# Kernel tuning notes

Measured on AMD Instinct MI355X. Metric: run time of the kernel, lower is better.

Reference implementation:

```python
import jax, jax.numpy as jnp
import numpy as np

D_IN = 1024
D_OUT = 1024
SEQ = 2048
BATCH = 4


def setup_inputs() -> dict:
    key = jax.random.key(0)
    ks = jax.random.split(key, 7)
    s_in = 1.0 / np.sqrt(D_IN)
    return {
        "x": jax.random.normal(ks[0], (BATCH, SEQ, D_IN), dtype=jnp.float32),
        "Wq": jax.random.normal(ks[1], (D_IN, D_OUT), dtype=jnp.float32) * s_in,
        "bq": jax.random.normal(ks[2], (D_OUT,), dtype=jnp.float32) * 0.01,
        "Wk": jax.random.normal(ks[3], (D_IN, D_OUT), dtype=jnp.float32) * s_in,
        "bk": jax.random.normal(ks[4], (D_OUT,), dtype=jnp.float32) * 0.01,
        "Wv": jax.random.normal(ks[5], (D_IN, D_OUT), dtype=jnp.float32) * s_in,
        "bv": jax.random.normal(ks[6], (D_OUT,), dtype=jnp.float32) * 0.01,
    }


def reference(x, Wq, bq, Wk, bk, Wv, bv):
    # x: [b, n, d_in]
    b, n, d_in = x.shape
    q = x @ Wq + bq  # [b, n, d_out]
    k = x @ Wk + bk
    v = x @ Wv + bv
    scale = 1.0 / jnp.sqrt(jnp.asarray(d_in, x.dtype))
    scores = jnp.einsum("bqd,bkd->bqk", q, k) * scale  # [b, n, n]
    causal = jnp.triu(jnp.ones((n, n), dtype=bool), k=1)  # True above diagonal
    scores = jnp.where(causal, -jnp.inf, scores)
    weights = jax.nn.softmax(scores, axis=-1)
    # dropout p=0.0 -> identity
    context = jnp.einsum("bqk,bkd->bqd", weights, v)
    return context
```

## Files before the change

### kernel.cpp

```cpp
#include <hip/hip_runtime.h>

typedef unsigned short u16;
typedef __bf16 bf16x8 __attribute__((ext_vector_type(8)));
typedef float floatx4 __attribute__((ext_vector_type(4)));

#define B_ 4
#define SEQ 2048
#define DIM 1024

__device__ __forceinline__ u16 f2bf(float f) {
    unsigned u = __builtin_bit_cast(unsigned, f);
    u += 0x7FFFu + ((u >> 16) & 1u);
    return (u16)(u >> 16);
}
__device__ __forceinline__ float bf2f(u16 h) {
    unsigned u = ((unsigned)h) << 16;
    return __builtin_bit_cast(float, u);
}

#define GPTR(p) ((const __attribute__((address_space(1))) void*)(p))
#define LPTR(p) ((__attribute__((address_space(3))) void*)(p))

__global__ __launch_bounds__(256) void convert_x(const float4* __restrict__ x,
                                                 ushort4* __restrict__ xb) {
    int i = blockIdx.x * 256 + threadIdx.x;
    float4 v = x[i];
    ushort4 o;
    o.x = f2bf(v.x); o.y = f2bf(v.y); o.z = f2bf(v.z); o.w = f2bf(v.w);
    xb[i] = o;
}

__global__ __launch_bounds__(256) void transpose_w(const float* __restrict__ Wq,
                                                   const float* __restrict__ Wk,
                                                   const float* __restrict__ Wv,
                                                   u16* __restrict__ Wt) {
    __shared__ u16 t[64][66];
    const int z = blockIdx.z;
    const float* W = (z == 0) ? Wq : ((z == 1) ? Wk : Wv);
    u16* out = Wt + (size_t)z * DIM * DIM;
    const int tx = threadIdx.x, ty = threadIdx.y;
    const int k0 = blockIdx.x * 64, n0 = blockIdx.y * 64;
#pragma unroll
    for (int j = 0; j < 8; j++) {
        int k = ty + 8 * j;
        float2 v = *(const float2*)(W + (size_t)(k0 + k) * DIM + n0 + 2 * tx);
        t[2 * tx][k] = f2bf(v.x);
        t[2 * tx + 1][k] = f2bf(v.y);
    }
    __syncthreads();
#pragma unroll
    for (int j = 0; j < 8; j++) {
        int n = ty + 8 * j;
        ushort2 o;
        o.x = t[n][2 * tx];
        o.y = t[n][2 * tx + 1];
        *(ushort2*)(out + (size_t)(n0 + n) * DIM + k0 + 2 * tx) = o;
    }
}

__device__ __forceinline__ void mainloop(
    const u16* __restrict__ Ab, const u16* __restrict__ Bb, int lda, int ldb,
    int Kt, u16* lsA, u16* lsB, int tid, int wave, int quad, int l15,
    int wm, int wn, floatx4 (&acc)[4][2]) {
    const int srow = tid >> 2;
    const int scol = ((tid & 3) ^ ((tid >> 3) & 3)) * 8;
    const u16* gA = Ab + (size_t)srow * lda + scol;
    const u16* gB = Bb + (size_t)srow * ldb + scol;
    const int swq = (quad ^ ((l15 >> 1) & 3)) * 8;
    const int rowA = l15 * 32;

#pragma unroll
    for (int i = 0; i < 4; i++)
#pragma unroll
        for (int j = 0; j < 2; j++) {
            floatx4 zz = {0.f, 0.f, 0.f, 0.f};
            acc[i][j] = zz;
        }

    for (int k0 = 0; k0 < Kt; k0 += 64) {
#pragma unroll
        for (int h = 0; h < 2; h++) {
            __builtin_amdgcn_global_load_lds(GPTR(gA + h * 32),
                LPTR(lsA + h * 4096 + wave * 512), 16, 0, 0);
            __builtin_amdgcn_global_load_lds(GPTR(gA + (size_t)64 * lda + h * 32),
                LPTR(lsA + h * 4096 + 2048 + wave * 512), 16, 0, 0);
            __builtin_amdgcn_global_load_lds(GPTR(gB + h * 32),
                LPTR(lsB + h * 2048 + wave * 512), 16, 0, 0);
        }
        gA += 64; gB += 64;
        __syncthreads();

#pragma unroll
        for (int h = 0; h < 2; h++) {
            bf16x8 af[4], bfr[2];
#pragma unroll
            for (int i = 0; i < 4; i++)
                af[i] = *(const bf16x8*)(lsA + h * 4096 + (wm + i * 16) * 32 + rowA + swq);
#pragma unroll
            for (int j = 0; j < 2; j++)
                bfr[j] = *(const bf16x8*)(lsB + h * 2048 + (wn + j * 16) * 32 + rowA + swq);
#pragma unroll
            for (int i = 0; i < 4; i++)
#pragma unroll
                for (int j = 0; j < 2; j++)
                    acc[i][j] = __builtin_amdgcn_mfma_f32_16x16x32_bf16(af[i], bfr[j], acc[i][j], 0, 0, 0);
        }
        __syncthreads();
    }
}

__global__ __launch_bounds__(256, 4) void gemm_qkv(
    const u16* __restrict__ A, const u16* __restrict__ Bt, u16* __restrict__ QK,
    const float* __restrict__ b0, const float* __restrict__ b1, const float* __restrict__ b2,
    u16* __restrict__ VtOut) {
    __shared__ union {
        struct { u16 a[128 * 64]; u16 b[64 * 64]; } stage;
        u16 epT[64 * 136];
    } sm;
    const int tid = threadIdx.x;
    const int wave = tid >> 6, lane = tid & 63;
    const int quad = lane >> 4, l15 = lane & 15;
    const int wm = (wave >> 1) * 64, wn = (wave & 1) * 32;
    const int z = blockIdx.x >> 4, xn = blockIdx.x & 15, yb = blockIdx.y;

    const u16* Ab = A + (size_t)yb * 128 * DIM;
    const u16* Bb = Bt + (size_t)z * DIM * DIM + (size_t)xn * 64 * DIM;
    floatx4 acc[4][2];
    mainloop(Ab, Bb, DIM, DIM, DIM, sm.stage.a, sm.stage.b,
             tid, wave, quad, l15, wm, wn, acc);

    const int colbase = xn * 64;
    const int mq = quad * 4;
    const float* bias = (z == 0) ? b0 : ((z == 1) ? b1 : b2);
    const int n0 = colbase + wn + l15;

    if (z < 2) {
        u16* Cb = QK + (size_t)z * B_ * SEQ * DIM;
        const int m0 = yb * 128 + wm + mq;
#pragma unroll
        for (int j = 0; j < 2; j++) {
            float bv_ = bias[n0 + j * 16];
#pragma unroll
            for (int i = 0; i < 4; i++)
#pragma unroll
                for (int r = 0; r < 4; r++)
                    Cb[(size_t)(m0 + i * 16 + r) * DIM + (n0 + j * 16)] = f2bf(acc[i][j][r] + bv_);
        }
        return;
    }

    float addj[2];
#pragma unroll
    for (int j = 0; j < 2; j++) addj[j] = bias[n0 + j * 16];
    __syncthreads();
#pragma unroll
    for (int i = 0; i < 4; i++)
#pragma unroll
        for (int j = 0; j < 2; j++)
#pragma unroll
            for (int r = 0; r < 4; r++) {
                int lr = wm + i * 16 + mq + r;
                int lc = wn + j * 16 + l15;
                sm.epT[lc * 136 + lr] = f2bf(acc[i][j][r] + addj[j]);
            }
    __syncthreads();
    const int b = (yb * 128) >> 11;
    const int sb = (yb * 128) & (SEQ - 1);
    u16* Vb = VtOut + (size_t)b * DIM * SEQ;
#pragma unroll
    for (int k = 0; k < 4; k++) {
        int s2 = tid + 256 * k;
        int n = s2 >> 4, seg = s2 & 15;
        uint4 val = *(const uint4*)&sm.epT[n * 136 + seg * 8];
        *(uint4*)(Vb + (size_t)(colbase + n) * SEQ + sb + seg * 8) = val;
    }
}

__global__ __launch_bounds__(256, 4) void gemm_scores(
    const u16* __restrict__ Q, const u16* __restrict__ K, u16* __restrict__ S,
    float scale) {
    const int ym = gridDim.y - 1 - blockIdx.y;
    if ((int)blockIdx.x > 2 * ym + 1) return;

    __shared__ u16 lsA[128 * 64];
    __shared__ u16 lsB[64 * 64];
    const int tid = threadIdx.x;
    const int wave = tid >> 6, lane = tid & 63;
    const int quad = lane >> 4, l15 = lane & 15;
    const int wm = (wave >> 1) * 64, wn = (wave & 1) * 32;
    const int z = blockIdx.z;

    const u16* Ab = Q + (size_t)z * SEQ * DIM + (size_t)ym * 128 * DIM;
    const u16* Bb = K + (size_t)z * SEQ * DIM + (size_t)blockIdx.x * 64 * DIM;
    floatx4 acc[4][2];
    mainloop(Ab, Bb, DIM, DIM, DIM, lsA, lsB,
             tid, wave, quad, l15, wm, wn, acc);

    u16* Cb = S + (size_t)z * SEQ * SEQ;
    const int m0 = ym * 128 + wm + quad * 4;
    const int n0 = blockIdx.x * 64 + wn + l15;
#pragma unroll
    for (int j = 0; j < 2; j++)
#pragma unroll
        for (int i = 0; i < 4; i++)
#pragma unroll
            for (int r = 0; r < 4; r++)
                Cb[(size_t)(m0 + i * 16 + r) * SEQ + (n0 + j * 16)] = f2bf(acc[i][j][r] * scale);
}

__global__ __launch_bounds__(256, 4) void gemm_pv(
    const u16* __restrict__ P, const u16* __restrict__ Vt, float* __restrict__ O) {
    const int ym = gridDim.y - 1 - blockIdx.y;
    __shared__ u16 lsA[128 * 64];
    __shared__ u16 lsB[64 * 64];
    const int tid = threadIdx.x;
    const int wave = tid >> 6, lane = tid & 63;
    const int quad = lane >> 4, l15 = lane & 15;
    const int wm = (wave >> 1) * 64, wn = (wave & 1) * 32;
    const int z = blockIdx.z;

    const u16* Ab = P + (size_t)z * SEQ * SEQ + (size_t)ym * 128 * SEQ;
    const u16* Bb = Vt + (size_t)z * DIM * SEQ + (size_t)blockIdx.x * 64 * SEQ;
    const int Kt = (ym + 1) * 128;
    floatx4 acc[4][2];
    mainloop(Ab, Bb, SEQ, SEQ, Kt, lsA, lsB,
             tid, wave, quad, l15, wm, wn, acc);

    float* Cf = O + (size_t)z * SEQ * DIM;
    const int m0 = ym * 128 + wm + quad * 4;
    const int n0 = blockIdx.x * 64 + wn + l15;
#pragma unroll
    for (int j = 0; j < 2; j++)
#pragma unroll
        for (int i = 0; i < 4; i++)
#pragma unroll
            for (int r = 0; r < 4; r++)
                Cf[(size_t)(m0 + i * 16 + r) * DIM + (n0 + j * 16)] = acc[i][j][r];
}

__global__ __launch_bounds__(256) void softmax_causal(u16* __restrict__ S) {
    const int q = blockIdx.x, b = blockIdx.y, tid = threadIdx.x;
    u16* row = S + ((size_t)b * SEQ + q) * SEQ;
    const int L = q + 1;
    const int Z = ((q >> 7) + 1) << 7;
    const int k0 = tid * 8;
    __shared__ float redm[4], reds[4];

    uint4 rv = ((const uint4*)row)[tid];
    unsigned w[4] = {rv.x, rv.y, rv.z, rv.w};
    float f[8];
#pragma unroll
    for (int e = 0; e < 8; e++) {
        u16 h = (u16)((w[e >> 1] >> ((e & 1) * 16)) & 0xFFFFu);
        f[e] = (k0 + e < L) ? bf2f(h) : -3.0e38f;
    }
    float m = f[0];
#pragma unroll
    for (int e = 1; e < 8; e++) m = fmaxf(m, f[e]);
#pragma unroll
    for (int o = 32; o > 0; o >>= 1) m = fmaxf(m, __shfl_xor(m, o));
    if ((tid & 63) == 0) redm[tid >> 6] = m;
    __syncthreads();
    m = fmaxf(fmaxf(redm[0], redm[1]), fmaxf(redm[2], redm[3]));

    float p[8];
    float s = 0.f;
#pragma unroll
    for (int e = 0; e < 8; e++) {
        p[e] = (k0 + e < L) ? __expf(f[e] - m) : 0.f;
        s += p[e];
    }
#pragma unroll
    for (int o = 32; o > 0; o >>= 1) s += __shfl_xor(s, o);
    if ((tid & 63) == 0) reds[tid >> 6] = s;
    __syncthreads();
    s = reds[0] + reds[1] + reds[2] + reds[3];
    const float inv = 1.0f / s;

    if (k0 < Z) {
        unsigned o2[4];
#pragma unroll
        for (int e = 0; e < 4; e++) {
            unsigned lo = f2bf(p[2 * e] * inv);
            unsigned hi = f2bf(p[2 * e + 1] * inv);
            o2[e] = lo | (hi << 16);
        }
        uint4 ov = {o2[0], o2[1], o2[2], o2[3]};
        ((uint4*)row)[tid] = ov;
    }
}

extern "C" void kernel_launch(void* const* d_in, const int* in_sizes, int n_in,
                              void* d_out, int out_size, void* d_ws, size_t ws_size,
                              hipStream_t stream) {
    const float* x = (const float*)d_in[0];
    const float* Wq = (const float*)d_in[1];
    const float* bq = (const float*)d_in[2];
    const float* Wk = (const float*)d_in[3];
    const float* bk = (const float*)d_in[4];
    const float* Wv = (const float*)d_in[5];
    const float* bv = (const float*)d_in[6];
    float* out = (float*)d_out;

    char* ws = (char*)d_ws;
    const size_t MB = 1024ull * 1024ull;
    u16* S = (u16*)ws;
    u16* xb = (u16*)ws;
    u16* Wt = (u16*)(ws + 16 * MB);
    u16* QK = (u16*)(ws + 32 * MB);
    u16* Vt = (u16*)(ws + 64 * MB);
    const size_t MAT = (size_t)B_ * SEQ * DIM;
    u16* Q = QK;
    u16* Km = QK + MAT;

    const float scale = 0.03125f;

    convert_x<<<8192, 256, 0, stream>>>((const float4*)x, (ushort4*)xb);
    transpose_w<<<dim3(16, 16, 3), dim3(32, 8), 0, stream>>>(Wq, Wk, Wv, Wt);
    gemm_qkv<<<dim3(48, 64), 256, 0, stream>>>(xb, Wt, QK, bq, bk, bv, Vt);
    gemm_scores<<<dim3(32, 16, 4), 256, 0, stream>>>(Q, Km, S, scale);
    softmax_causal<<<dim3(SEQ, B_), 256, 0, stream>>>(S);
    gemm_pv<<<dim3(16, 16, 4), 256, 0, stream>>>(S, Vt, out);
}
```

Measured before the change: 282.6 us.

## Enlarge GEMM block tiles to 128x128 with 64x64 per-wave subtiles

All three GEMM kernels move from 128x64 block tiles to 128x128, with each wave computing a 64x64 output subtile (4x4 MFMA accumulators) instead of 64x32. The aim is to raise arithmetic intensity per LDS and global load and halve the number of blocks. The cost is more registers, hence launch bounds lowered to 3 blocks per CU, and larger LDS B buffers. The V-transpose epilogue is split into two passes so it still fits the existing shared buffer.

Result: faster. 249.6 us (-11.7%).

```diff
diff --git a/kernel.cpp b/kernel.cpp
--- a/kernel.cpp
+++ b/kernel.cpp
@@ -61,75 +61,75 @@
 __device__ __forceinline__ void mainloop(
     const u16* __restrict__ Ab, const u16* __restrict__ Bb, int lda, int ldb,
     int Kt, u16* lsA, u16* lsB, int tid, int wave, int quad, int l15,
-    int wm, int wn, floatx4 (&acc)[4][2]) {
+    int wm, int wn, floatx4 (&acc)[4][4]) {
     const int srow = tid >> 2;
     const int scol = ((tid & 3) ^ ((tid >> 3) & 3)) * 8;
     const u16* gA = Ab + (size_t)srow * lda + scol;
     const u16* gB = Bb + (size_t)srow * ldb + scol;
     const int swq = (quad ^ ((l15 >> 1) & 3)) * 8;
-    const int rowA = l15 * 32;
 
 #pragma unroll
     for (int i = 0; i < 4; i++)
 #pragma unroll
-        for (int j = 0; j < 2; j++) {
+        for (int j = 0; j < 4; j++) {
             floatx4 zz = {0.f, 0.f, 0.f, 0.f};
             acc[i][j] = zz;
         }
 
     for (int k0 = 0; k0 < Kt; k0 += 64) {
 #pragma unroll
-        for (int h = 0; h < 2; h++) {
-            __builtin_amdgcn_global_load_lds(GPTR(gA + h * 32),
-                LPTR(lsA + h * 4096 + wave * 512), 16, 0, 0);
-            __builtin_amdgcn_global_load_lds(GPTR(gA + (size_t)64 * lda + h * 32),
-                LPTR(lsA + h * 4096 + 2048 + wave * 512), 16, 0, 0);
-            __builtin_amdgcn_global_load_lds(GPTR(gB + h * 32),
-                LPTR(lsB + h * 2048 + wave * 512), 16, 0, 0);
-        }
+        for (int h = 0; h < 2; h++)
+#pragma unroll
+            for (int c = 0; c < 2; c++) {
+                __builtin_amdgcn_global_load_lds(
+                    GPTR(gA + (size_t)c * 64 * lda + h * 32),
+                    LPTR(lsA + h * 4096 + c * 2048 + wave * 512), 16, 0, 0);
+                __builtin_amdgcn_global_load_lds(
+                    GPTR(gB + (size_t)c * 64 * ldb + h * 32),
+                    LPTR(lsB + h * 4096 + c * 2048 + wave * 512), 16, 0, 0);
+            }
         gA += 64; gB += 64;
         __syncthreads();
 
 #pragma unroll
         for (int h = 0; h < 2; h++) {
-            bf16x8 af[4], bfr[2];
+            bf16x8 af[4];
 #pragma unroll
             for (int i = 0; i < 4; i++)
-                af[i] = *(const bf16x8*)(lsA + h * 4096 + (wm + i * 16) * 32 + rowA + swq);
-#pragma unroll
-            for (int j = 0; j < 2; j++)
-                bfr[j] = *(const bf16x8*)(lsB + h * 2048 + (wn + j * 16) * 32 + rowA + swq);
-#pragma unroll
-            for (int i = 0; i < 4; i++)
-#pragma unroll
-                for (int j = 0; j < 2; j++)
-                    acc[i][j] = __builtin_amdgcn_mfma_f32_16x16x32_bf16(af[i], bfr[j], acc[i][j], 0, 0, 0);
+                af[i] = *(const bf16x8*)(lsA + h * 4096 + (wm + i * 16 + l15) * 32 + swq);
+#pragma unroll
+            for (int j = 0; j < 4; j++) {
+                bf16x8 bfr = *(const bf16x8*)(lsB + h * 4096 + (wn + j * 16 + l15) * 32 + swq);
+#pragma unroll
+                for (int i = 0; i < 4; i++)
+                    acc[i][j] = __builtin_amdgcn_mfma_f32_16x16x32_bf16(af[i], bfr, acc[i][j], 0, 0, 0);
+            }
         }
         __syncthreads();
     }
 }
 
-__global__ __launch_bounds__(256, 4) void gemm_qkv(
+__global__ __launch_bounds__(256, 3) void gemm_qkv(
     const u16* __restrict__ A, const u16* __restrict__ Bt, u16* __restrict__ QK,
     const float* __restrict__ b0, const float* __restrict__ b1, const float* __restrict__ b2,
     u16* __restrict__ VtOut) {
     __shared__ union {
-        struct { u16 a[128 * 64]; u16 b[64 * 64]; } stage;
+        struct { u16 a[128 * 64]; u16 b[128 * 64]; } stage;
         u16 epT[64 * 136];
     } sm;
     const int tid = threadIdx.x;
     const int wave = tid >> 6, lane = tid & 63;
     const int quad = lane >> 4, l15 = lane & 15;
-    const int wm = (wave >> 1) * 64, wn = (wave & 1) * 32;
-    const int z = blockIdx.x >> 4, xn = blockIdx.x & 15, yb = blockIdx.y;
+    const int wm = (wave >> 1) * 64, wn = (wave & 1) * 64;
+    const int z = blockIdx.x >> 3, xn = blockIdx.x & 7, yb = blockIdx.y;
 
     const u16* Ab = A + (size_t)yb * 128 * DIM;
-    const u16* Bb = Bt + (size_t)z * DIM * DIM + (size_t)xn * 64 * DIM;
-    floatx4 acc[4][2];
+    const u16* Bb = Bt + (size_t)z * DIM * DIM + (size_t)xn * 128 * DIM;
+    floatx4 acc[4][4];
     mainloop(Ab, Bb, DIM, DIM, DIM, sm.stage.a, sm.stage.b,
              tid, wave, quad, l15, wm, wn, acc);
 
-    const int colbase = xn * 64;
+    const int colbase = xn * 128;
     const int mq = quad * 4;
     const float* bias = (z == 0) ? b0 : ((z == 1) ? b1 : b2);
     const int n0 = colbase + wn + l15;
@@ -138,7 +138,7 @@
         u16* Cb = QK + (size_t)z * B_ * SEQ * DIM;
         const int m0 = yb * 128 + wm + mq;
 #pragma unroll
-        for (int j = 0; j < 2; j++) {
+        for (int j = 0; j < 4; j++) {
             float bv_ = bias[n0 + j * 16];
 #pragma unroll
             for (int i = 0; i < 4; i++)
@@ -149,58 +149,63 @@
         return;
     }
 
-    float addj[2];
-#pragma unroll
-    for (int j = 0; j < 2; j++) addj[j] = bias[n0 + j * 16];
-    __syncthreads();
-#pragma unroll
-    for (int i = 0; i < 4; i++)
-#pragma unroll
-        for (int j = 0; j < 2; j++)
-#pragma unroll
-            for (int r = 0; r < 4; r++) {
-                int lr = wm + i * 16 + mq + r;
-                int lc = wn + j * 16 + l15;
-                sm.epT[lc * 136 + lr] = f2bf(acc[i][j][r] + addj[j]);
-            }
-    __syncthreads();
+    float addj[4];
+#pragma unroll
+    for (int j = 0; j < 4; j++) addj[j] = bias[n0 + j * 16];
     const int b = (yb * 128) >> 11;
     const int sb = (yb * 128) & (SEQ - 1);
     u16* Vb = VtOut + (size_t)b * DIM * SEQ;
 #pragma unroll
-    for (int k = 0; k < 4; k++) {
-        int s2 = tid + 256 * k;
-        int n = s2 >> 4, seg = s2 & 15;
-        uint4 val = *(const uint4*)&sm.epT[n * 136 + seg * 8];
-        *(uint4*)(Vb + (size_t)(colbase + n) * SEQ + sb + seg * 8) = val;
-    }
-}
-
-__global__ __launch_bounds__(256, 4) void gemm_scores(
+    for (int c = 0; c < 2; c++) {
+        __syncthreads();
+        if ((wave & 1) == c) {
+#pragma unroll
+            for (int i = 0; i < 4; i++)
+#pragma unroll
+                for (int j = 0; j < 4; j++)
+#pragma unroll
+                    for (int r = 0; r < 4; r++) {
+                        int lr = wm + i * 16 + mq + r;
+                        int lc = j * 16 + l15;
+                        sm.epT[lc * 136 + lr] = f2bf(acc[i][j][r] + addj[j]);
+                    }
+        }
+        __syncthreads();
+#pragma unroll
+        for (int k = 0; k < 4; k++) {
+            int s2 = tid + 256 * k;
+            int n = s2 >> 4, seg = s2 & 15;
+            uint4 val = *(const uint4*)&sm.epT[n * 136 + seg * 8];
+            *(uint4*)(Vb + (size_t)(colbase + c * 64 + n) * SEQ + sb + seg * 8) = val;
+        }
+    }
+}
+
+__global__ __launch_bounds__(256, 3) void gemm_scores(
     const u16* __restrict__ Q, const u16* __restrict__ K, u16* __restrict__ S,
     float scale) {
     const int ym = gridDim.y - 1 - blockIdx.y;
-    if ((int)blockIdx.x > 2 * ym + 1) return;
+    if ((int)blockIdx.x > ym) return;
 
     __shared__ u16 lsA[128 * 64];
-    __shared__ u16 lsB[64 * 64];
+    __shared__ u16 lsB[128 * 64];
     const int tid = threadIdx.x;
     const int wave = tid >> 6, lane = tid & 63;
     const int quad = lane >> 4, l15 = lane & 15;
-    const int wm = (wave >> 1) * 64, wn = (wave & 1) * 32;
+    const int wm = (wave >> 1) * 64, wn = (wave & 1) * 64;
     const int z = blockIdx.z;
 
     const u16* Ab = Q + (size_t)z * SEQ * DIM + (size_t)ym * 128 * DIM;
-    const u16* Bb = K + (size_t)z * SEQ * DIM + (size_t)blockIdx.x * 64 * DIM;
-    floatx4 acc[4][2];
+    const u16* Bb = K + (size_t)z * SEQ * DIM + (size_t)blockIdx.x * 128 * DIM;
+    floatx4 acc[4][4];
     mainloop(Ab, Bb, DIM, DIM, DIM, lsA, lsB,
              tid, wave, quad, l15, wm, wn, acc);
 
     u16* Cb = S + (size_t)z * SEQ * SEQ;
     const int m0 = ym * 128 + wm + quad * 4;
-    const int n0 = blockIdx.x * 64 + wn + l15;
-#pragma unroll
-    for (int j = 0; j < 2; j++)
+    const int n0 = blockIdx.x * 128 + wn + l15;
+#pragma unroll
+    for (int j = 0; j < 4; j++)
 #pragma unroll
         for (int i = 0; i < 4; i++)
 #pragma unroll
@@ -208,29 +213,29 @@
                 Cb[(size_t)(m0 + i * 16 + r) * SEQ + (n0 + j * 16)] = f2bf(acc[i][j][r] * scale);
 }
 
-__global__ __launch_bounds__(256, 4) void gemm_pv(
+__global__ __launch_bounds__(256, 3) void gemm_pv(
     const u16* __restrict__ P, const u16* __restrict__ Vt, float* __restrict__ O) {
     const int ym = gridDim.y - 1 - blockIdx.y;
     __shared__ u16 lsA[128 * 64];
-    __shared__ u16 lsB[64 * 64];
+    __shared__ u16 lsB[128 * 64];
     const int tid = threadIdx.x;
     const int wave = tid >> 6, lane = tid & 63;
     const int quad = lane >> 4, l15 = lane & 15;
-    const int wm = (wave >> 1) * 64, wn = (wave & 1) * 32;
+    const int wm = (wave >> 1) * 64, wn = (wave & 1) * 64;
     const int z = blockIdx.z;
 
     const u16* Ab = P + (size_t)z * SEQ * SEQ + (size_t)ym * 128 * SEQ;
-    const u16* Bb = Vt + (size_t)z * DIM * SEQ + (size_t)blockIdx.x * 64 * SEQ;
+    const u16* Bb = Vt + (size_t)z * DIM * SEQ + (size_t)blockIdx.x * 128 * SEQ;
     const int Kt = (ym + 1) * 128;
-    floatx4 acc[4][2];
+    floatx4 acc[4][4];
     mainloop(Ab, Bb, SEQ, SEQ, Kt, lsA, lsB,
              tid, wave, quad, l15, wm, wn, acc);
 
     float* Cf = O + (size_t)z * SEQ * DIM;
     const int m0 = ym * 128 + wm + quad * 4;
-    const int n0 = blockIdx.x * 64 + wn + l15;
-#pragma unroll
-    for (int j = 0; j < 2; j++)
+    const int n0 = blockIdx.x * 128 + wn + l15;
+#pragma unroll
+    for (int j = 0; j < 4; j++)
 #pragma unroll
         for (int i = 0; i < 4; i++)
 #pragma unroll
@@ -317,8 +322,8 @@
 
     convert_x<<<8192, 256, 0, stream>>>((const float4*)x, (ushort4*)xb);
     transpose_w<<<dim3(16, 16, 3), dim3(32, 8), 0, stream>>>(Wq, Wk, Wv, Wt);
-    gemm_qkv<<<dim3(48, 64), 256, 0, stream>>>(xb, Wt, QK, bq, bk, bv, Vt);
-    gemm_scores<<<dim3(32, 16, 4), 256, 0, stream>>>(Q, Km, S, scale);
+    gemm_qkv<<<dim3(24, 64), 256, 0, stream>>>(xb, Wt, QK, bq, bk, bv, Vt);
+    gemm_scores<<<dim3(16, 16, 4), 256, 0, stream>>>(Q, Km, S, scale);
     softmax_causal<<<dim3(SEQ, B_), 256, 0, stream>>>(S);
-    gemm_pv<<<dim3(16, 16, 4), 256, 0, stream>>>(S, Vt, out);
-}
+    gemm_pv<<<dim3(8, 16, 4), 256, 0, stream>>>(S, Vt, out);
+}
```
